# Kernel optimization log

Measured on AMD Instinct MI355X. Metric: run time of the kernel, lower is better.

## Reference

```python
import jax, jax.numpy as jnp
import numpy as np

N_HEAD = 16

def setup_inputs() -> dict:
    key = jax.random.key(0)
    ks = jax.random.split(key, 9)
    B, T, C = 4, 2048, 1024
    s = 0.02
    return {
        "x": jax.random.normal(ks[0], (B, T, C), dtype=jnp.float32),
        "Wq": jax.random.normal(ks[1], (C, C), dtype=jnp.float32) * s,
        "bq": jnp.zeros((C,), dtype=jnp.float32),
        "Wk": jax.random.normal(ks[2], (C, C), dtype=jnp.float32) * s,
        "bk": jnp.zeros((C,), dtype=jnp.float32),
        "Wv": jax.random.normal(ks[3], (C, C), dtype=jnp.float32) * s,
        "bv": jnp.zeros((C,), dtype=jnp.float32),
        "Wo": jax.random.normal(ks[4], (C, C), dtype=jnp.float32) * s,
        "bo": jnp.zeros((C,), dtype=jnp.float32),
    }

def reference(x, Wq, bq, Wk, bk, Wv, bv, Wo, bo):
    B, T, C = x.shape
    H = N_HEAD
    d = C // H
    # QKV projections (Linear: y = x @ W + b), split heads -> [B, H, T, d]
    def proj(W, b):
        return (x @ W + b).reshape(B, T, H, d).transpose(0, 2, 1, 3)
    q = proj(Wq, bq)
    k = proj(Wk, bk)
    v = proj(Wv, bv)
    scale = jnp.float32(d) ** -0.5
    scores = jnp.einsum("bhtd,bhsd->bhts", q, k) * scale  # [B,H,T,T]
    attn = jax.nn.softmax(scores, axis=-1)
    out = jnp.einsum("bhts,bhsd->bhtd", attn, v)  # [B,H,T,d]
    out = out.transpose(0, 2, 1, 3).reshape(B, T, C)
    return out @ Wo + bo
```

## Files before the change

### kernel.cpp

```cpp
#include <hip/hip_runtime.h>
#include <hip/hip_bf16.h>

typedef unsigned short u16;
typedef unsigned int   u32;

typedef __bf16 bf16x8 __attribute__((ext_vector_type(8)));
typedef float  f32x4  __attribute__((ext_vector_type(4)));

#define MFMA16(A, B, C) __builtin_amdgcn_mfma_f32_16x16x32_bf16(A, B, C, 0, 0, 0)

static __device__ __forceinline__ u16 f2bf(float f) {
  union { float f; u32 u; } v; v.f = f;
  u32 r = v.u + 0x7fffu + ((v.u >> 16) & 1u);
  return (u16)(r >> 16);
}

static __device__ __forceinline__ float exp2a(float x) {
  float r; asm("v_exp_f32 %0, %1" : "=v"(r) : "v"(x)); return r;
}
static __device__ __forceinline__ float max3f(float a, float b, float c) {
  float r; asm("v_max3_f32 %0, %1, %2, %3" : "=v"(r) : "v"(a), "v"(b), "v"(c)); return r;
}
static __device__ __forceinline__ u32 cvtpk(float lo, float hi) {
  u32 r; asm("v_cvt_pk_bf16_f32 %0, %1, %2" : "=v"(r) : "v"(lo), "v"(hi)); return r;
}

static __device__ __forceinline__ void async16(const void* g, void* l) {
  __builtin_amdgcn_global_load_lds((const __attribute__((address_space(1))) void*)g,
                                   (__attribute__((address_space(3))) void*)l, 16, 0, 0);
}

static __device__ __forceinline__ int permrow(int r) {
  return (r & 3) | (((r >> 3) & 1) << 2);
}

__global__ __launch_bounds__(256) void cvtx_k(const float* __restrict__ x, u16* __restrict__ xb) {
  size_t i = ((size_t)blockIdx.x * 256 + threadIdx.x) * 4;
  float4 v = *(const float4*)(x + i);
  u32 lo = (u32)f2bf(v.x) | ((u32)f2bf(v.y) << 16);
  u32 hi = (u32)f2bf(v.z) | ((u32)f2bf(v.w) << 16);
  *(uint2*)(xb + i) = make_uint2(lo, hi);
}

__global__ __launch_bounds__(256) void wt_k(const float* __restrict__ Wq, const float* __restrict__ Wk,
                                            const float* __restrict__ Wv, const float* __restrict__ Wo,
                                            u16* __restrict__ WT) {
  const int z = blockIdx.z;
  const float* W = (z == 0) ? Wq : (z == 1) ? Wk : (z == 2) ? Wv : Wo;
  u16* out = WT + (size_t)z * 1048576;
  __shared__ float tile[32][33];
  const int tx = threadIdx.x & 31, ty = threadIdx.x >> 5;
  const int n0 = blockIdx.x * 32, k0 = blockIdx.y * 32;
#pragma unroll
  for (int i = 0; i < 4; i++)
    tile[ty + i * 8][tx] = W[(size_t)(k0 + ty + i * 8) * 1024 + n0 + tx];
  __syncthreads();
#pragma unroll
  for (int i = 0; i < 4; i++)
    out[(size_t)(n0 + ty + i * 8) * 1024 + k0 + tx] = f2bf(tile[tx][ty + i * 8]);
}

template <int MODE>
__global__ __launch_bounds__(256) void gemm_k(const u16* __restrict__ A, const u16* __restrict__ WTall,
                                              const float* __restrict__ b0, const float* __restrict__ b1,
                                              const float* __restrict__ b2,
                                              u16* __restrict__ outb, float* __restrict__ outf) {
  __shared__ u16 As[128 * 32];
  __shared__ u16 Bs[128 * 32];
  const int tid = threadIdx.x;
  const int m0 = blockIdx.x * 128;
  const int n0 = blockIdx.y * 128;
  const int z = blockIdx.z;
  const u16* WT = WTall + (size_t)(MODE == 0 ? z : 3) * 1048576;
  const float* bias = (MODE == 0) ? (z == 0 ? b0 : (z == 1 ? b1 : b2)) : b0;
  const float scl = (MODE == 0 && z == 0) ? 0.18033688011112042f : 1.0f;

  const int lane = tid & 63;
  const int wid = tid >> 6;
  const int wr = wid >> 1, wc = wid & 1;
  const int g = lane >> 4, cc = lane & 15;

  const int srow = tid >> 2;
  const int scol = (tid & 3) * 8;
  const u16* gA0 = A + (size_t)(m0 + srow) * 1024 + scol;
  const u16* gA1 = A + (size_t)(m0 + srow + 64) * 1024 + scol;
  const u16* gB0 = WT + (size_t)(n0 + srow) * 1024 + scol;
  const u16* gB1 = WT + (size_t)(n0 + srow + 64) * 1024 + scol;
  u16* lA0 = &As[tid * 8]; u16* lA1 = &As[2048 + tid * 8];
  u16* lB0 = &Bs[tid * 8]; u16* lB1 = &Bs[2048 + tid * 8];

  f32x4 acc[4][4] = {};

  for (int kb = 0; kb < 1024; kb += 32) {
    __syncthreads();
    async16(gA0 + kb, lA0);
    async16(gA1 + kb, lA1);
    async16(gB0 + kb, lB0);
    async16(gB1 + kb, lB1);
    __syncthreads();
    bf16x8 af[4], bfv[4];
#pragma unroll
    for (int i = 0; i < 4; i++)
      af[i] = *(const bf16x8*)&As[(wr * 64 + i * 16 + cc) * 32 + g * 8];
#pragma unroll
    for (int i = 0; i < 4; i++)
      bfv[i] = *(const bf16x8*)&Bs[(wc * 64 + i * 16 + cc) * 32 + g * 8];
#pragma unroll
    for (int mi = 0; mi < 4; mi++)
#pragma unroll
      for (int ni = 0; ni < 4; ni++)
        acc[mi][ni] = MFMA16(af[mi], bfv[ni], acc[mi][ni]);
  }

#pragma unroll
  for (int mi = 0; mi < 4; mi++) {
#pragma unroll
    for (int ni = 0; ni < 4; ni++) {
      const int n = n0 + wc * 64 + ni * 16 + cc;
      const float bn = bias[n];
      const int mb = m0 + wr * 64 + mi * 16 + g * 4;
      if (MODE == 0) {
        u16* o = outb + (size_t)z * 8388608;
        if (z == 2) {
          u16 h[4];
#pragma unroll
          for (int r = 0; r < 4; r++) h[r] = f2bf(acc[mi][ni][r] + bn);
          const size_t idx = ((size_t)(((mb >> 11) * 16 + (n >> 6)) * 64 + (n & 63))) * 2048 + (mb & 2047);
          *(uint2*)&o[idx] = make_uint2((u32)h[0] | ((u32)h[1] << 16), (u32)h[2] | ((u32)h[3] << 16));
        } else {
#pragma unroll
          for (int r = 0; r < 4; r++) {
            const int m = mb + r;
            const float val = (acc[mi][ni][r] + bn) * scl;
            o[((size_t)((m >> 11) * 16 + (n >> 6)) * 2048 + (m & 2047)) * 64 + (n & 63)] = f2bf(val);
          }
        }
      } else {
#pragma unroll
        for (int r = 0; r < 4; r++)
          outf[(size_t)(mb + r) * 1024 + n] = acc[mi][ni][r] + bn;
      }
    }
  }
}

#define SMAX(S0, S1, PF)                                                      \
  {                                                                           \
    float pm_ = max3f(max3f(S0[0], S0[1], S0[2]),                             \
                      max3f(S0[3], S1[0], S1[1]), fmaxf(S1[2], S1[3]));       \
    if (__builtin_expect(!__all(pm_ <= m_run + 8.0f), 0)) {                   \
      pm_ = fmaxf(pm_, __shfl_xor(pm_, 16));                                  \
      pm_ = fmaxf(pm_, __shfl_xor(pm_, 32));                                  \
      const float mn_ = fmaxf(m_run, pm_);                                    \
      const float al_ = exp2a(m_run - mn_);                                   \
      _Pragma("unroll")                                                       \
      for (int r_ = 0; r_ < 4; ++r_) {                                        \
        const float ar_ = __shfl(al_, g * 4 + r_);                            \
        _Pragma("unroll")                                                     \
        for (int t_ = 0; t_ < 5; ++t_) o[t_][r_] *= ar_;                      \
      }                                                                       \
      m_run = mn_;                                                            \
    }                                                                         \
    const float e0_ = exp2a(S0[0] - m_run), e1_ = exp2a(S0[1] - m_run);       \
    const float e2_ = exp2a(S0[2] - m_run), e3_ = exp2a(S0[3] - m_run);       \
    const float e4_ = exp2a(S1[0] - m_run), e5_ = exp2a(S1[1] - m_run);       \
    const float e6_ = exp2a(S1[2] - m_run), e7_ = exp2a(S1[3] - m_run);       \
    union { u32 u[4]; bf16x8 v; } pu_;                                        \
    pu_.u[0] = cvtpk(e0_, e1_); pu_.u[1] = cvtpk(e2_, e3_);                   \
    pu_.u[2] = cvtpk(e4_, e5_); pu_.u[3] = cvtpk(e6_, e7_);                   \
    PF = pu_.v;                                                               \
  }

#define COMPUTE(BUF)                                                          \
  _Pragma("unroll")                                                           \
  for (int sub = 0; sub < 2; ++sub) {                                         \
    const u16* pV_ = sub ? pV1 : pV0;                                         \
    bf16x8 k00 = *(const bf16x8*)(pK0 + (BUF)*4096 + sub*2048 + 0*256);       \
    bf16x8 k01 = *(const bf16x8*)(pK1 + (BUF)*4096 + sub*2048 + 0*256);       \
    bf16x8 k10 = *(const bf16x8*)(pK0 + (BUF)*4096 + sub*2048 + 1*256);       \
    bf16x8 k11 = *(const bf16x8*)(pK1 + (BUF)*4096 + sub*2048 + 1*256);       \
    __builtin_amdgcn_s_setprio(1);                                            \
    f32x4 s0 = {}, s1 = {};                                                   \
    s0 = MFMA16(k00, qf[0], s0); s0 = MFMA16(k01, qf[1], s0);                 \
    s1 = MFMA16(k10, qf[0], s1); s1 = MFMA16(k11, qf[1], s1);                 \
    __builtin_amdgcn_s_setprio(0);                                            \
    bf16x8 pf;                                                                \
    SMAX(s0, s1, pf);                                                         \
    __builtin_amdgcn_s_setprio(1);                                            \
    _Pragma("unroll")                                                         \
    for (int t = 0; t < 4; ++t) {                                             \
      bf16x8 vf = *(const bf16x8*)(pV_ + (BUF)*4096 + t*1024);                \
      o[t] = MFMA16(pf, vf, o[t]);                                            \
    }                                                                         \
    o[4] = MFMA16(pf, vone, o[4]);                                            \
    __builtin_amdgcn_s_setprio(0);                                            \
  }

#define STEP(BUF, IT)                                                         \
  {                                                                           \
    __syncthreads();                                                          \
    if ((IT) < 31) {                                                          \
      const size_t ko_ = (size_t)((IT) + 1) * 4096;                           \
      const size_t vo_ = (size_t)((IT) + 1) * 64;                             \
      async16(kS0 + ko_, &Ks[((BUF) ^ 1) * 4096 + tid * 8]);                  \
      async16(kS1 + ko_, &Ks[((BUF) ^ 1) * 4096 + tid * 8 + 2048]);           \
      async16(vS0 + vo_, &Vs[((BUF) ^ 1) * 4096 + tid * 8]);                  \
      async16(vS1 + vo_, &Vs[((BUF) ^ 1) * 4096 + tid * 8 + 2048]);           \
    }                                                                         \
    COMPUTE(BUF)                                                              \
  }

__global__ __launch_bounds__(256) void attn_k(const u16* __restrict__ Qg, const u16* __restrict__ Kg,
                                              const u16* __restrict__ Vtg, u16* __restrict__ ctx) {
  __shared__ u16 Ks[8192];
  __shared__ u16 Vs[8192];
  const int tid = threadIdx.x;
  const int lane = tid & 63;
  const int wid = tid >> 6;
  const int g = lane >> 4, cc = lane & 15;
  const int a_ = cc >> 2, b_ = cc & 3;

  const int bid = blockIdx.x;
  const int xcd = bid & 7, tt = bid >> 3;
  const int bh = xcd * 8 + (tt >> 5);
  const int q0 = (tt & 31) * 64 + wid * 16;
  const size_t base = (size_t)bh * 131072;

  bf16x8 qf[2];
#pragma unroll
  for (int c2 = 0; c2 < 2; c2++)
    qf[c2] = *(const bf16x8*)(Qg + base + (size_t)(q0 + cc) * 64 + c2 * 32 + g * 8);

  bf16x8 vone;
#pragma unroll
  for (int j = 0; j < 8; j++) vone[j] = (__bf16)1.0f;

  float m_run = -30000.0f;
  f32x4 o[5] = {};

  const int cK = b_ | ((a_ & 1) << 2);
  const int slK = g ^ cK;
  const u16* pK0 = &Ks[(8 * a_ + b_) * 64 + (slK << 3)];
  const u16* pK1 = &Ks[(8 * a_ + b_) * 64 + ((slK ^ 4) << 3)];
  const int cV = b_ | (((cc >> 3) & 1) << 2);
  const u16* pV0 = &Vs[cc * 64 + ((g ^ cV) << 3)];
  const u16* pV1 = &Vs[cc * 64 + (((4 + g) ^ cV) << 3)];

  const int r0 = tid >> 3, r1 = r0 + 32;
  const int slot = tid & 7;
  const int sp0 = slot ^ permrow(r0), sp1 = slot ^ permrow(r1);
  const u16* kS0 = Kg + base + (size_t)r0 * 64 + (sp0 << 3);
  const u16* kS1 = Kg + base + (size_t)r1 * 64 + (sp1 << 3);
  const u16* vS0 = Vtg + base + (size_t)r0 * 2048 + (sp0 << 3);
  const u16* vS1 = Vtg + base + (size_t)r1 * 2048 + (sp1 << 3);

  async16(kS0, &Ks[tid * 8]);
  async16(kS1, &Ks[tid * 8 + 2048]);
  async16(vS0, &Vs[tid * 8]);
  async16(vS1, &Vs[tid * 8 + 2048]);

  for (int it = 0; it < 32; it += 2) {
    STEP(0, it)
    STEP(1, it + 1)
  }

  const int b = bh >> 4, h = bh & 15;
#pragma unroll
  for (int r = 0; r < 4; r++) {
    const float inv = __builtin_amdgcn_rcpf(o[4][r]);
    const int q = q0 + g * 4 + r;
#pragma unroll
    for (int t = 0; t < 4; t++)
      ctx[((size_t)((b * 2048 + q) * 16 + h)) * 64 + t * 16 + cc] = f2bf(o[t][r] * inv);
  }
}

extern "C" void kernel_launch(void* const* d_in, const int* in_sizes, int n_in,
                              void* d_out, int out_size, void* d_ws, size_t ws_size,
                              hipStream_t stream) {
  const float* x  = (const float*)d_in[0];
  const float* Wq = (const float*)d_in[1];
  const float* bq = (const float*)d_in[2];
  const float* Wk = (const float*)d_in[3];
  const float* bk = (const float*)d_in[4];
  const float* Wv = (const float*)d_in[5];
  const float* bv = (const float*)d_in[6];
  const float* Wo = (const float*)d_in[7];
  const float* bo = (const float*)d_in[8];
  float* out = (float*)d_out;

  char* w = (char*)d_ws;
  u16* xb   = (u16*)(w);
  u16* WT   = (u16*)(w + (16u << 20));
  u16* QKV  = (u16*)(w + (24u << 20));
  u16* ctxb = (u16*)(w + (72u << 20));

  cvtx_k<<<dim3(8192), dim3(256), 0, stream>>>(x, xb);
  wt_k<<<dim3(32, 32, 4), dim3(256), 0, stream>>>(Wq, Wk, Wv, Wo, WT);
  gemm_k<0><<<dim3(64, 8, 3), dim3(256), 0, stream>>>(xb, WT, bq, bk, bv, QKV, nullptr);
  attn_k<<<dim3(2048), dim3(256), 0, stream>>>(QKV, QKV + 8388608, QKV + 2 * 8388608, ctxb);
  gemm_k<1><<<dim3(64, 8, 1), dim3(256), 0, stream>>>(ctxb, WT, bo, nullptr, nullptr, nullptr, out);
}
```

Measured before the change: 217.2 us.

## Halve attention KV tile to 32 keys and raise occupancy to 8 blocks

```diff
diff --git a/kernel.cpp b/kernel.cpp
--- a/kernel.cpp
+++ b/kernel.cpp
@@ -172,13 +172,11 @@
   }
 
 #define COMPUTE(BUF)                                                          \
-  _Pragma("unroll")                                                           \
-  for (int sub = 0; sub < 2; ++sub) {                                         \
-    const u16* pV_ = sub ? pV1 : pV0;                                         \
-    bf16x8 k00 = *(const bf16x8*)(pK0 + (BUF)*4096 + sub*2048 + 0*256);       \
-    bf16x8 k01 = *(const bf16x8*)(pK1 + (BUF)*4096 + sub*2048 + 0*256);       \
-    bf16x8 k10 = *(const bf16x8*)(pK0 + (BUF)*4096 + sub*2048 + 1*256);       \
-    bf16x8 k11 = *(const bf16x8*)(pK1 + (BUF)*4096 + sub*2048 + 1*256);       \
+  {                                                                           \
+    bf16x8 k00 = *(const bf16x8*)(pK0 + (BUF)*2048);                          \
+    bf16x8 k01 = *(const bf16x8*)(pK1 + (BUF)*2048);                          \
+    bf16x8 k10 = *(const bf16x8*)(pK0 + (BUF)*2048 + 256);                    \
+    bf16x8 k11 = *(const bf16x8*)(pK1 + (BUF)*2048 + 256);                    \
     __builtin_amdgcn_s_setprio(1);                                            \
     f32x4 s0 = {}, s1 = {};                                                   \
     s0 = MFMA16(k00, qf[0], s0); s0 = MFMA16(k01, qf[1], s0);                 \
@@ -189,7 +187,8 @@
     __builtin_amdgcn_s_setprio(1);                                            \
     _Pragma("unroll")                                                         \
     for (int t = 0; t < 4; ++t) {                                             \
-      bf16x8 vf = *(const bf16x8*)(pV_ + (BUF)*4096 + t*1024);                \
+      const u16* pV_ = (t & 1) ? pV1 : pV0;                                   \
+      bf16x8 vf = *(const bf16x8*)(pV_ + (BUF)*2048 + t * 512);               \
       o[t] = MFMA16(pf, vf, o[t]);                                            \
     }                                                                         \
     o[4] = MFMA16(pf, vone, o[4]);                                            \
@@ -199,21 +198,17 @@
 #define STEP(BUF, IT)                                                         \
   {                                                                           \
     __syncthreads();                                                          \
-    if ((IT) < 31) {                                                          \
-      const size_t ko_ = (size_t)((IT) + 1) * 4096;                           \
-      const size_t vo_ = (size_t)((IT) + 1) * 64;                             \
-      async16(kS0 + ko_, &Ks[((BUF) ^ 1) * 4096 + tid * 8]);                  \
-      async16(kS1 + ko_, &Ks[((BUF) ^ 1) * 4096 + tid * 8 + 2048]);           \
-      async16(vS0 + vo_, &Vs[((BUF) ^ 1) * 4096 + tid * 8]);                  \
-      async16(vS1 + vo_, &Vs[((BUF) ^ 1) * 4096 + tid * 8 + 2048]);           \
+    if ((IT) < 63) {                                                          \
+      async16(kS + (size_t)((IT) + 1) * 2048, &Ks[((BUF) ^ 1) * 2048 + tid * 8]); \
+      async16(vS + (size_t)((IT) + 1) * 32,   &Vs[((BUF) ^ 1) * 2048 + tid * 8]); \
     }                                                                         \
     COMPUTE(BUF)                                                              \
   }
 
-__global__ __launch_bounds__(256) void attn_k(const u16* __restrict__ Qg, const u16* __restrict__ Kg,
-                                              const u16* __restrict__ Vtg, u16* __restrict__ ctx) {
-  __shared__ u16 Ks[8192];
-  __shared__ u16 Vs[8192];
+__global__ __launch_bounds__(256, 8) void attn_k(const u16* __restrict__ Qg, const u16* __restrict__ Kg,
+                                                 const u16* __restrict__ Vtg, u16* __restrict__ ctx) {
+  __shared__ u16 Ks[2 * 2048];
+  __shared__ u16 Vs[2 * 2048];
   const int tid = threadIdx.x;
   const int lane = tid & 63;
   const int wid = tid >> 6;
@@ -242,24 +237,19 @@
   const int slK = g ^ cK;
   const u16* pK0 = &Ks[(8 * a_ + b_) * 64 + (slK << 3)];
   const u16* pK1 = &Ks[(8 * a_ + b_) * 64 + ((slK ^ 4) << 3)];
-  const int cV = b_ | (((cc >> 3) & 1) << 2);
-  const u16* pV0 = &Vs[cc * 64 + ((g ^ cV) << 3)];
-  const u16* pV1 = &Vs[cc * 64 + (((4 + g) ^ cV) << 3)];
-
-  const int r0 = tid >> 3, r1 = r0 + 32;
-  const int slot = tid & 7;
-  const int sp0 = slot ^ permrow(r0), sp1 = slot ^ permrow(r1);
-  const u16* kS0 = Kg + base + (size_t)r0 * 64 + (sp0 << 3);
-  const u16* kS1 = Kg + base + (size_t)r1 * 64 + (sp1 << 3);
-  const u16* vS0 = Vtg + base + (size_t)r0 * 2048 + (sp0 << 3);
-  const u16* vS1 = Vtg + base + (size_t)r1 * 2048 + (sp1 << 3);
-
-  async16(kS0, &Ks[tid * 8]);
-  async16(kS1, &Ks[tid * 8 + 2048]);
-  async16(vS0, &Vs[tid * 8]);
-  async16(vS1, &Vs[tid * 8 + 2048]);
-
-  for (int it = 0; it < 32; it += 2) {
+  const int sV = (((cc & 1) << 2) | g) ^ ((cc >> 1) & 3);
+  const u16* pV0 = &Vs[(cc >> 1) * 64 + (sV << 3)];
+  const u16* pV1 = &Vs[(cc >> 1) * 64 + ((sV ^ 4) << 3)];
+
+  const int ln = tid >> 3;
+  const int sp = (tid & 7) ^ permrow(ln);
+  const u16* kS = Kg + base + (size_t)ln * 64 + (sp << 3);
+  const u16* vS = Vtg + base + (size_t)(2 * ln + (sp >> 2)) * 2048 + ((sp & 3) << 3);
+
+  async16(kS, &Ks[tid * 8]);
+  async16(vS, &Vs[tid * 8]);
+
+  for (int it = 0; it < 64; it += 2) {
     STEP(0, it)
     STEP(1, it + 1)
   }
```

Result: faster. 211.1 us (-2.8%).
